# Performance work log

Hardware: AMD Instinct MI355X
Metric: run time of the kernel (lower is better)

The kernel has to match this reference:

```python
import jax, jax.numpy as jnp
import numpy as np

N_NODES = 100000

def gcn_conv(x, W, b, src, dst):
    n = x.shape[0]
    loop = jnp.arange(n, dtype=src.dtype)
    src_f = jnp.concatenate([src, loop])
    dst_f = jnp.concatenate([dst, loop])
    deg = jax.ops.segment_sum(jnp.ones_like(src_f, dtype=x.dtype), dst_f, num_segments=n)
    dinv = jnp.where(deg > 0, deg ** -0.5, 0.0)
    norm = dinv[src_f] * dinv[dst_f]              # [E+N]
    h = x @ W                                      # [N, out]
    msg = h[src_f] * norm[:, None]                 # gather + scale
    out = jax.ops.segment_sum(msg, dst_f, num_segments=n)
    return out + b

def setup_inputs() -> dict:
    key = jax.random.key(0)
    k1, k2, k3, k4, k5 = jax.random.split(key, 5)
    d = 128
    x = jax.random.normal(k1, (N_NODES, d), dtype=jnp.float32)
    e = jax.random.randint(k2, (2, 3200000), 0, N_NODES, dtype=jnp.int64)
    # Glorot-style init as in PyG GCNConv
    W1 = jax.random.normal(k3, (d, 64), dtype=jnp.float32) * (1.0 / np.sqrt(d))
    b1 = jnp.zeros((64,), dtype=jnp.float32)
    W2 = jax.random.normal(k4, (64, 1), dtype=jnp.float32) * (1.0 / np.sqrt(64))
    b2 = jnp.zeros((1,), dtype=jnp.float32)
    return {"x": x, "e": e, "W1": W1, "b1": b1, "W2": W2, "b2": b2}

def reference(x, e, W1, b1, W2, b2):
    src, dst = e[0], e[1]
    h = jax.nn.relu(gcn_conv(x, W1, b1, src, dst))
    return gcn_conv(h, W2, b2, src, dst)
```

## Files before the change

### kernel.cpp

```cpp
#include <hip/hip_runtime.h>
#include <hip/hip_bf16.h>


typedef short s8_t __attribute__((ext_vector_type(8)));
typedef float f4_t __attribute__((ext_vector_type(4)));

__device__ __forceinline__ float bf2f(unsigned short u) {
    union { unsigned int u; float f; } c; c.u = ((unsigned int)u) << 16; return c.f;
}
__device__ __forceinline__ unsigned short f2bf(float f) {
    union { float f; unsigned int u; } c; c.f = f;
    unsigned int u = c.u;
    unsigned int r = (u + 0x7fffu + ((u >> 16) & 1u)) >> 16;
    return (unsigned short)r;
}
__device__ __forceinline__ float loadF(const void* p, int i, int isbf) {
    return isbf ? bf2f(((const unsigned short*)p)[i]) : ((const float*)p)[i];
}
__device__ __forceinline__ int edgeIdx(const void* e, long long i, int is64) {
    return is64 ? (int)((const long long*)e)[i] : ((const int*)e)[i];
}

__global__ void k_detect_prep(const void* e, const void* x, const void* W1,
                              int* flags, unsigned short* __restrict__ wT,
                              unsigned short* __restrict__ wTh,
                              unsigned short* __restrict__ wTl) {
    __shared__ int sfl;
    int tid = threadIdx.x;
    if (tid < 64) {
        unsigned int ew = ((const unsigned int*)e)[2 * tid + 1];
        unsigned long long nz = __ballot(ew != 0);
        unsigned int xw = ((const unsigned int*)x)[tid];
        unsigned int low = xw & 0xffffu;
        unsigned int e8 = (low >> 7) & 0xffu;
        bool plaus = (low == 0u) || (e8 >= 110u && e8 <= 135u);
        unsigned long long pl = __ballot(plaus);
        if (tid == 0) {
            flags[0] = (nz == 0ull) ? 1 : 0;
            int isbf = (__popcll(pl) > 32) ? 1 : 0;
            flags[1] = isbf;
            sfl = isbf;
        }
    }
    __syncthreads();
    int isbf = sfl;
    if (isbf) {
        const unsigned short* w = (const unsigned short*)W1;
        for (int idx = tid; idx < 128 * 64; idx += 256) {
            int k = idx >> 6, n = idx & 63;
            wT[n * 128 + k] = w[idx];
        }
    } else {
        const float* w = (const float*)W1;
        for (int idx = tid; idx < 128 * 64; idx += 256) {
            int k = idx >> 6, n = idx & 63;
            float v = w[idx];
            unsigned short h = f2bf(v);
            wTh[n * 128 + k] = h;
            wTl[n * 128 + k] = f2bf(v - bf2f(h));
        }
    }
}

__launch_bounds__(256)
__global__ void k_hist(const void* e, int* __restrict__ histT, const int* flags,
                       int E, int B, int HB) {
    __shared__ int hist[1024];
    int tid = threadIdx.x;
    int is64 = flags[0];
    for (int f = tid; f < B; f += 256) hist[f] = 0;
    __syncthreads();
    int base = blockIdx.x * 4096;
    #pragma unroll
    for (int k = 0; k < 16; ++k) {
        int i = base + k * 256 + tid;
        if (i < E) {
            int d = edgeIdx(e, (long long)E + i, is64);
            atomicAdd(&hist[d >> 9], 1);
        }
    }
    __syncthreads();
    for (int f = tid; f < B; f += 256)
        histT[(long long)f * HB + blockIdx.x] = hist[f];
}

__global__ void k_scanA(int* __restrict__ data, int* __restrict__ partial, int M) {
    __shared__ int s[256];
    int tid = threadIdx.x;
    int i = blockIdx.x * 256 + tid;
    int v = (i < M) ? data[i] : 0;
    s[tid] = v; __syncthreads();
    for (int off = 1; off < 256; off <<= 1) {
        int t = (tid >= off) ? s[tid - off] : 0;
        __syncthreads(); s[tid] += t; __syncthreads();
    }
    if (i < M) data[i] = s[tid] - v;
    if (tid == 255) partial[blockIdx.x] = s[255];
}

__global__ void k_scanC(int* __restrict__ data, const int* __restrict__ partial,
                        int* __restrict__ bucketStart, int M, int HB, int B, int E) {
    __shared__ int red[256];
    int tid = threadIdx.x;
    int bb = blockIdx.x;
    int s = 0;
    for (int j = tid; j < bb; j += 256) s += partial[j];
    red[tid] = s; __syncthreads();
    for (int off = 128; off > 0; off >>= 1) {
        if (tid < off) red[tid] += red[tid + off];
        __syncthreads();
    }
    int base = red[0];
    int f = bb * 256 + tid;
    if (f < M) {
        int val = data[f] + base;
        data[f] = val;
        int q = f / HB;
        if (f - q * HB == 0) bucketStart[q] = val;
    }
    if (f == 0) bucketStart[B] = E;
}

__launch_bounds__(256)
__global__ void k_part(const void* e, const int* __restrict__ histT,
                       int* __restrict__ part, const int* flags,
                       int E, int B, int HB) {
    __shared__ int lcur[1024];
    __shared__ int lcnt[1024];
    __shared__ int sc[256];
    __shared__ int buf[4096];
    __shared__ unsigned short bkt[4096];
    int tid = threadIdx.x;
    int is64 = flags[0];
    for (int f = tid; f < 1024; f += 256) {
        lcur[f] = (f < B) ? histT[(long long)f * HB + blockIdx.x] : 0;
        lcnt[f] = 0;
    }
    __syncthreads();
    int base = blockIdx.x * 4096;
    int val[16], bk[16], rk[16];
    #pragma unroll
    for (int k = 0; k < 16; ++k) {
        int i = base + k * 256 + tid;
        if (i < E) {
            int s = edgeIdx(e, i, is64);
            int d = edgeIdx(e, (long long)E + i, is64);
            val[k] = s | ((d & 511) << 17);
            bk[k] = d >> 9;
            rk[k] = atomicAdd(&lcnt[bk[k]], 1);
        } else {
            bk[k] = -1;
        }
    }
    __syncthreads();
    int c0 = lcnt[4 * tid], c1 = lcnt[4 * tid + 1];
    int c2 = lcnt[4 * tid + 2], c3 = lcnt[4 * tid + 3];
    int tot = c0 + c1 + c2 + c3;
    sc[tid] = tot; __syncthreads();
    for (int off = 1; off < 256; off <<= 1) {
        int t = (tid >= off) ? sc[tid - off] : 0;
        __syncthreads(); sc[tid] += t; __syncthreads();
    }
    int run = sc[tid] - tot;
    lcnt[4 * tid]     = run;
    lcnt[4 * tid + 1] = run + c0;
    lcnt[4 * tid + 2] = run + c0 + c1;
    lcnt[4 * tid + 3] = run + c0 + c1 + c2;
    __syncthreads();
    #pragma unroll
    for (int k = 0; k < 16; ++k) {
        if (bk[k] >= 0) {
            int slot = lcnt[bk[k]] + rk[k];
            buf[slot] = val[k];
            bkt[slot] = (unsigned short)bk[k];
        }
    }
    __syncthreads();
    int total = E - base; if (total > 4096) total = 4096;
    for (int t = tid; t < total; t += 256) {
        int bb = bkt[t];
        part[lcur[bb] + (t - lcnt[bb])] = buf[t];
    }
}

__launch_bounds__(512)
__global__ void k_sort2(const int* __restrict__ part, const int* __restrict__ bucketStart,
                        int* __restrict__ srcSorted, int* __restrict__ start,
                        float* __restrict__ dinv, int N, int B) {
    __shared__ int cnt[512];
    __shared__ int s[512];
    __shared__ int cur[512];
    int tid = threadIdx.x, b = blockIdx.x;
    cnt[tid] = 0;
    __syncthreads();
    int lo = bucketStart[b], hi = bucketStart[b + 1];
    for (int idx = lo + tid; idx < hi; idx += 512)
        atomicAdd(&cnt[(part[idx] >> 17) & 511], 1);
    __syncthreads();
    int v = cnt[tid];
    s[tid] = v; __syncthreads();
    for (int off = 1; off < 512; off <<= 1) {
        int t = (tid >= off) ? s[tid - off] : 0;
        __syncthreads(); s[tid] += t; __syncthreads();
    }
    int base_ = lo + s[tid] - v;
    cur[tid] = base_;
    int node = b * 512 + tid;
    if (node < N) {
        start[node] = base_;
        dinv[node] = rsqrtf((float)(v + 1));
    }
    if (b == 0 && tid == 0) start[N] = bucketStart[B];
    __syncthreads();
    for (int idx = lo + tid; idx < hi; idx += 512) {
        int pw = part[idx];
        int pos = atomicAdd(&cur[(pw >> 17) & 511], 1);
        srcSorted[pos] = pw & 0x1FFFF;
    }
}

__launch_bounds__(256)
__global__ void k_gemm(const void* x, const unsigned short* __restrict__ wT,
                       const unsigned short* __restrict__ wTh,
                       const unsigned short* __restrict__ wTl,
                       const float* __restrict__ dinv,
                       unsigned short* __restrict__ hb, const int* flags, int N) {
    int tid = threadIdx.x;
    int lane = tid & 63, wv = tid >> 6;
    int q = lane >> 4, r = lane & 15;
    int gw = blockIdx.x * 4 + wv;
    int nW = gridDim.x * 4;
    int RB = (N + 15) >> 4;
    int isbf = flags[1];
    if (isbf) {
        const unsigned short* xb = (const unsigned short*)x;
        for (int rb = gw; rb < RB; rb += nW) {
            int row0 = rb * 16;
            int arow = row0 + r;
            s8_t a[4];
            #pragma unroll
            for (int kk = 0; kk < 4; ++kk)
                a[kk] = (arow < N)
                    ? *(const s8_t*)&xb[(long long)arow * 128 + kk * 32 + q * 8]
                    : (s8_t)(short)0;
            f4_t acc[4];
            #pragma unroll
            for (int nt = 0; nt < 4; ++nt) acc[nt] = (f4_t){0.f, 0.f, 0.f, 0.f};
            #pragma unroll
            for (int nt = 0; nt < 4; ++nt) {
                #pragma unroll
                for (int kk = 0; kk < 4; ++kk) {
                    s8_t b = *(const s8_t*)&wT[(nt * 16 + r) * 128 + kk * 32 + q * 8];
                    acc[nt] = __builtin_amdgcn_mfma_f32_16x16x32_bf16(a[kk], b, acc[nt], 0, 0, 0);
                }
            }
            #pragma unroll
            for (int reg = 0; reg < 4; ++reg) {
                int row = row0 + q * 4 + reg;
                if (row < N) {
                    float dv = dinv[row];
                    #pragma unroll
                    for (int nt = 0; nt < 4; ++nt)
                        hb[(long long)row * 64 + nt * 16 + r] = f2bf(acc[nt][reg] * dv);
                }
            }
        }
    } else {
        const float* xf = (const float*)x;
        f4_t cx0[4], cx1[4];
        int rb = gw;
        if (rb < RB) {
            int arow = rb * 16 + r;
            #pragma unroll
            for (int kk = 0; kk < 4; ++kk) {
                if (arow < N) {
                    const float* p = &xf[(long long)arow * 128 + kk * 32 + q * 8];
                    cx0[kk] = *(const f4_t*)p;
                    cx1[kk] = *(const f4_t*)(p + 4);
                } else {
                    cx0[kk] = (f4_t){0.f, 0.f, 0.f, 0.f};
                    cx1[kk] = (f4_t){0.f, 0.f, 0.f, 0.f};
                }
            }
        }
        for (; rb < RB; rb += nW) {
            s8_t ah[4], al[4];
            #pragma unroll
            for (int kk = 0; kk < 4; ++kk) {
                #pragma unroll
                for (int j = 0; j < 4; ++j) {
                    union { float f; unsigned int u; } c0, h0, r0, c1, h1, r1;
                    c0.f = cx0[kk][j];
                    h0.u = c0.u & 0xffff0000u;
                    ah[kk][j] = (short)(c0.u >> 16);
                    r0.f = c0.f - h0.f;
                    al[kk][j] = (short)(r0.u >> 16);
                    c1.f = cx1[kk][j];
                    h1.u = c1.u & 0xffff0000u;
                    ah[kk][4 + j] = (short)(c1.u >> 16);
                    r1.f = c1.f - h1.f;
                    al[kk][4 + j] = (short)(r1.u >> 16);
                }
            }
            int rbn = rb + nW;
            if (rbn < RB) {
                int arow = rbn * 16 + r;
                #pragma unroll
                for (int kk = 0; kk < 4; ++kk) {
                    if (arow < N) {
                        const float* p = &xf[(long long)arow * 128 + kk * 32 + q * 8];
                        cx0[kk] = *(const f4_t*)p;
                        cx1[kk] = *(const f4_t*)(p + 4);
                    } else {
                        cx0[kk] = (f4_t){0.f, 0.f, 0.f, 0.f};
                        cx1[kk] = (f4_t){0.f, 0.f, 0.f, 0.f};
                    }
                }
            }
            f4_t acc[4];
            #pragma unroll
            for (int nt = 0; nt < 4; ++nt) acc[nt] = (f4_t){0.f, 0.f, 0.f, 0.f};
            #pragma unroll
            for (int nt = 0; nt < 4; ++nt) {
                #pragma unroll
                for (int kk = 0; kk < 4; ++kk) {
                    s8_t bh = *(const s8_t*)&wTh[(nt * 16 + r) * 128 + kk * 32 + q * 8];
                    s8_t bl = *(const s8_t*)&wTl[(nt * 16 + r) * 128 + kk * 32 + q * 8];
                    acc[nt] = __builtin_amdgcn_mfma_f32_16x16x32_bf16(ah[kk], bh, acc[nt], 0, 0, 0);
                    acc[nt] = __builtin_amdgcn_mfma_f32_16x16x32_bf16(al[kk], bh, acc[nt], 0, 0, 0);
                    acc[nt] = __builtin_amdgcn_mfma_f32_16x16x32_bf16(ah[kk], bl, acc[nt], 0, 0, 0);
                }
            }
            int row0 = rb * 16;
            #pragma unroll
            for (int reg = 0; reg < 4; ++reg) {
                int row = row0 + q * 4 + reg;
                if (row < N) {
                    float dv = dinv[row];
                    #pragma unroll
                    for (int nt = 0; nt < 4; ++nt)
                        hb[(long long)row * 64 + nt * 16 + r] = f2bf(acc[nt][reg] * dv);
                }
            }
        }
    }
}

__launch_bounds__(256)
__global__ void k_agg1(const unsigned short* __restrict__ hb,
                       const float* __restrict__ dinv,
                       const int* __restrict__ start,
                       const int* __restrict__ srcSorted,
                       const void* b1, const void* W2, float* __restrict__ sbuf2,
                       const int* flags, int N) {
    int lane = threadIdx.x & 63;
    int node = (blockIdx.x * blockDim.x + threadIdx.x) >> 6;
    if (node >= N) return;
    int isbf = flags[1];
    float di = dinv[node];
    int base = start[node], cnt = start[node + 1] - base;
    float acc = bf2f(hb[(long long)node * 64 + lane]);
    for (int c = 0; c < cnt; c += 64) {
        int t = c + lane;
        int sidx = (t < cnt) ? srcSorted[base + t] : 0;
        int m = cnt - c; if (m > 64) m = 64;
        int t2 = 0;
        for (; t2 + 16 <= m; t2 += 16) {
            int s0  = __shfl(sidx, t2 + 0),  s1  = __shfl(sidx, t2 + 1);
            int s2  = __shfl(sidx, t2 + 2),  s3  = __shfl(sidx, t2 + 3);
            int s4  = __shfl(sidx, t2 + 4),  s5  = __shfl(sidx, t2 + 5);
            int s6  = __shfl(sidx, t2 + 6),  s7  = __shfl(sidx, t2 + 7);
            int s8  = __shfl(sidx, t2 + 8),  s9  = __shfl(sidx, t2 + 9);
            int s10 = __shfl(sidx, t2 + 10), s11 = __shfl(sidx, t2 + 11);
            int s12 = __shfl(sidx, t2 + 12), s13 = __shfl(sidx, t2 + 13);
            int s14 = __shfl(sidx, t2 + 14), s15 = __shfl(sidx, t2 + 15);
            unsigned short v0  = hb[(long long)s0  * 64 + lane];
            unsigned short v1  = hb[(long long)s1  * 64 + lane];
            unsigned short v2  = hb[(long long)s2  * 64 + lane];
            unsigned short v3  = hb[(long long)s3  * 64 + lane];
            unsigned short v4  = hb[(long long)s4  * 64 + lane];
            unsigned short v5  = hb[(long long)s5  * 64 + lane];
            unsigned short v6  = hb[(long long)s6  * 64 + lane];
            unsigned short v7  = hb[(long long)s7  * 64 + lane];
            unsigned short v8  = hb[(long long)s8  * 64 + lane];
            unsigned short v9  = hb[(long long)s9  * 64 + lane];
            unsigned short v10 = hb[(long long)s10 * 64 + lane];
            unsigned short v11 = hb[(long long)s11 * 64 + lane];
            unsigned short v12 = hb[(long long)s12 * 64 + lane];
            unsigned short v13 = hb[(long long)s13 * 64 + lane];
            unsigned short v14 = hb[(long long)s14 * 64 + lane];
            unsigned short v15 = hb[(long long)s15 * 64 + lane];
            acc += bf2f(v0);  acc += bf2f(v1);  acc += bf2f(v2);  acc += bf2f(v3);
            acc += bf2f(v4);  acc += bf2f(v5);  acc += bf2f(v6);  acc += bf2f(v7);
            acc += bf2f(v8);  acc += bf2f(v9);  acc += bf2f(v10); acc += bf2f(v11);
            acc += bf2f(v12); acc += bf2f(v13); acc += bf2f(v14); acc += bf2f(v15);
        }
        for (; t2 + 8 <= m; t2 += 8) {
            int s0 = __shfl(sidx, t2 + 0), s1 = __shfl(sidx, t2 + 1);
            int s2 = __shfl(sidx, t2 + 2), s3 = __shfl(sidx, t2 + 3);
            int s4 = __shfl(sidx, t2 + 4), s5 = __shfl(sidx, t2 + 5);
            int s6 = __shfl(sidx, t2 + 6), s7 = __shfl(sidx, t2 + 7);
            unsigned short v0 = hb[(long long)s0 * 64 + lane];
            unsigned short v1 = hb[(long long)s1 * 64 + lane];
            unsigned short v2 = hb[(long long)s2 * 64 + lane];
            unsigned short v3 = hb[(long long)s3 * 64 + lane];
            unsigned short v4 = hb[(long long)s4 * 64 + lane];
            unsigned short v5 = hb[(long long)s5 * 64 + lane];
            unsigned short v6 = hb[(long long)s6 * 64 + lane];
            unsigned short v7 = hb[(long long)s7 * 64 + lane];
            acc += bf2f(v0); acc += bf2f(v1); acc += bf2f(v2); acc += bf2f(v3);
            acc += bf2f(v4); acc += bf2f(v5); acc += bf2f(v6); acc += bf2f(v7);
        }
        for (; t2 < m; ++t2) {
            int s0 = __shfl(sidx, t2);
            acc += bf2f(hb[(long long)s0 * 64 + lane]);
        }
    }
    float v = acc * di + loadF(b1, lane, isbf);
    v = fmaxf(v, 0.f);
    float p = v * loadF(W2, lane, isbf);
    #pragma unroll
    for (int o = 32; o >= 1; o >>= 1) p += __shfl_xor(p, o);
    if (lane == 0) sbuf2[node] = p * di;
}

__launch_bounds__(256)
__global__ void k_agg2(const float* __restrict__ sbuf2, const float* __restrict__ dinv,
                       const int* __restrict__ start,
                       const int* __restrict__ srcSorted,
                       const void* b2, void* out, const int* flags, int N) {
    int lane = threadIdx.x & 63;
    int node = (blockIdx.x * blockDim.x + threadIdx.x) >> 6;
    if (node >= N) return;
    int isbf = flags[1];
    float di = dinv[node];
    int base = start[node], cnt = start[node + 1] - base;
    float part = 0.f;
    for (int t = lane; t < cnt; t += 64) part += sbuf2[srcSorted[base + t]];
    #pragma unroll
    for (int o = 32; o >= 1; o >>= 1) part += __shfl_xor(part, o);
    if (lane == 0) {
        float o_ = (part + sbuf2[node]) * di + loadF(b2, 0, isbf);
        if (isbf) ((unsigned short*)out)[node] = f2bf(o_);
        else      ((float*)out)[node] = o_;
    }
}

extern "C" void kernel_launch(void* const* d_in, const int* in_sizes, int n_in,
                              void* d_out, int out_size, void* d_ws, size_t ws_size,
                              hipStream_t stream) {
    const void* x  = d_in[0];
    const void* e  = d_in[1];
    const void* W1 = d_in[2];
    const void* b1 = d_in[3];
    const void* W2 = d_in[4];
    const void* b2 = d_in[5];
    int N = in_sizes[0] / 128;
    int E = in_sizes[1] / 2;
    int B  = (N + 511) / 512;
    int HB = (E + 4095) / 4096;
    int M  = B * HB;
    int nP = (M + 255) / 256;
    int NB = B * 512;
    int EP = ((E + 255) / 256) * 256;

    int*   wsI         = (int*)d_ws;
    int*   flags       = wsI;
    unsigned short* wT  = (unsigned short*)(wsI + 256);
    unsigned short* wTh = (unsigned short*)(wsI + 256 + 4096);
    unsigned short* wTl = (unsigned short*)(wsI + 256 + 8192);
    int*   histT       = wsI + 256 + 12288;
    int*   partial     = histT + ((M + 255) / 256) * 256;
    int*   bucketStart = partial + ((nP + 255) / 256) * 256;
    float* dinv        = (float*)(bucketStart + 1040);
    float* sbuf2       = dinv + NB;
    int*   start       = (int*)(sbuf2 + NB);
    int*   srcSorted   = start + NB + 256;
    int*   part        = srcSorted + EP;
    unsigned short* hb = (unsigned short*)part;

    hipLaunchKernelGGL(k_detect_prep, dim3(1), dim3(256), 0, stream,
                       e, x, W1, flags, wT, wTh, wTl);
    hipLaunchKernelGGL(k_hist, dim3(HB), dim3(256), 0, stream, e, histT, flags, E, B, HB);
    hipLaunchKernelGGL(k_scanA, dim3(nP), dim3(256), 0, stream, histT, partial, M);
    hipLaunchKernelGGL(k_scanC, dim3(nP), dim3(256), 0, stream,
                       histT, partial, bucketStart, M, HB, B, E);
    hipLaunchKernelGGL(k_part, dim3(HB), dim3(256), 0, stream, e, histT, part, flags, E, B, HB);
    hipLaunchKernelGGL(k_sort2, dim3(B), dim3(512), 0, stream,
                       part, bucketStart, srcSorted, start, dinv, N, B);
    hipLaunchKernelGGL(k_gemm, dim3(512), dim3(256), 0, stream,
                       x, wT, wTh, wTl, dinv, hb, flags, N);
    hipLaunchKernelGGL(k_agg1, dim3((N + 3) / 4), dim3(256), 0, stream,
                       hb, dinv, start, srcSorted, b1, W2, sbuf2, flags, N);
    hipLaunchKernelGGL(k_agg2, dim3((N + 3) / 4), dim3(256), 0, stream,
                       sbuf2, dinv, start, srcSorted, b2, d_out, flags, N);
}
```

Measured before the change: 297.8 us.

## Replace global histogram+scan partition with local-sorted chunks and binary-search gather

Removes the separate histogram pass over dst and the two-kernel global scan. Each partition block now sorts its 4096-edge chunk by bucket locally, writes it back in place, and records per-bucket offsets and counts. A per-bucket reduction produces bucket totals, and the sort kernel binary-searches the chunk offsets to gather its bucket's edges from every chunk. This avoids one full read of the edge array and two launches, but the sort kernel now does scattered reads with a binary search over about 782 chunks per element, twice.

```diff
diff --git a/kernel.cpp b/kernel.cpp
--- a/kernel.cpp
+++ b/kernel.cpp
@@ -63,79 +63,15 @@
 }
 
 __launch_bounds__(256)
-__global__ void k_hist(const void* e, int* __restrict__ histT, const int* flags,
-                       int E, int B, int HB) {
-    __shared__ int hist[1024];
-    int tid = threadIdx.x;
-    int is64 = flags[0];
-    for (int f = tid; f < B; f += 256) hist[f] = 0;
-    __syncthreads();
-    int base = blockIdx.x * 4096;
-    #pragma unroll
-    for (int k = 0; k < 16; ++k) {
-        int i = base + k * 256 + tid;
-        if (i < E) {
-            int d = edgeIdx(e, (long long)E + i, is64);
-            atomicAdd(&hist[d >> 9], 1);
-        }
-    }
-    __syncthreads();
-    for (int f = tid; f < B; f += 256)
-        histT[(long long)f * HB + blockIdx.x] = hist[f];
-}
-
-__global__ void k_scanA(int* __restrict__ data, int* __restrict__ partial, int M) {
-    __shared__ int s[256];
-    int tid = threadIdx.x;
-    int i = blockIdx.x * 256 + tid;
-    int v = (i < M) ? data[i] : 0;
-    s[tid] = v; __syncthreads();
-    for (int off = 1; off < 256; off <<= 1) {
-        int t = (tid >= off) ? s[tid - off] : 0;
-        __syncthreads(); s[tid] += t; __syncthreads();
-    }
-    if (i < M) data[i] = s[tid] - v;
-    if (tid == 255) partial[blockIdx.x] = s[255];
-}
-
-__global__ void k_scanC(int* __restrict__ data, const int* __restrict__ partial,
-                        int* __restrict__ bucketStart, int M, int HB, int B, int E) {
-    __shared__ int red[256];
-    int tid = threadIdx.x;
-    int bb = blockIdx.x;
-    int s = 0;
-    for (int j = tid; j < bb; j += 256) s += partial[j];
-    red[tid] = s; __syncthreads();
-    for (int off = 128; off > 0; off >>= 1) {
-        if (tid < off) red[tid] += red[tid + off];
-        __syncthreads();
-    }
-    int base = red[0];
-    int f = bb * 256 + tid;
-    if (f < M) {
-        int val = data[f] + base;
-        data[f] = val;
-        int q = f / HB;
-        if (f - q * HB == 0) bucketStart[q] = val;
-    }
-    if (f == 0) bucketStart[B] = E;
-}
-
-__launch_bounds__(256)
-__global__ void k_part(const void* e, const int* __restrict__ histT,
-                       int* __restrict__ part, const int* flags,
-                       int E, int B, int HB) {
-    __shared__ int lcur[1024];
+__global__ void k_part2(const void* e, int* __restrict__ histT,
+                        int* __restrict__ histC, int* __restrict__ part,
+                        const int* flags, int E, int B, int HB) {
     __shared__ int lcnt[1024];
     __shared__ int sc[256];
     __shared__ int buf[4096];
-    __shared__ unsigned short bkt[4096];
     int tid = threadIdx.x;
     int is64 = flags[0];
-    for (int f = tid; f < 1024; f += 256) {
-        lcur[f] = (f < B) ? histT[(long long)f * HB + blockIdx.x] : 0;
-        lcnt[f] = 0;
-    }
+    for (int f = tid; f < 1024; f += 256) lcnt[f] = 0;
     __syncthreads();
     int base = blockIdx.x * 4096;
     int val[16], bk[16], rk[16];
@@ -168,34 +104,80 @@
     lcnt[4 * tid + 3] = run + c0 + c1 + c2;
     __syncthreads();
     #pragma unroll
-    for (int k = 0; k < 16; ++k) {
-        if (bk[k] >= 0) {
-            int slot = lcnt[bk[k]] + rk[k];
-            buf[slot] = val[k];
-            bkt[slot] = (unsigned short)bk[k];
-        }
-    }
-    __syncthreads();
+    for (int k = 0; k < 16; ++k)
+        if (bk[k] >= 0) buf[lcnt[bk[k]] + rk[k]] = val[k];
+    __syncthreads();
+    for (int f = tid; f < B; f += 256) {
+        int st = lcnt[f], en = lcnt[f + 1];
+        histT[(long long)f * HB + blockIdx.x] = st;
+        histC[(long long)f * HB + blockIdx.x] = en - st;
+    }
     int total = E - base; if (total > 4096) total = 4096;
-    for (int t = tid; t < total; t += 256) {
-        int bb = bkt[t];
-        part[lcur[bb] + (t - lcnt[bb])] = buf[t];
-    }
+    for (int t = tid; t < total; t += 256) part[base + t] = buf[t];
+}
+
+__launch_bounds__(256)
+__global__ void k_bstart(const int* __restrict__ histC,
+                         int* __restrict__ bucketTotal, int HB) {
+    __shared__ int red[256];
+    int tid = threadIdx.x, b = blockIdx.x;
+    int s = 0;
+    for (int j = tid; j < HB; j += 256) s += histC[(long long)b * HB + j];
+    red[tid] = s; __syncthreads();
+    for (int off = 128; off > 0; off >>= 1) {
+        if (tid < off) red[tid] += red[tid + off];
+        __syncthreads();
+    }
+    if (tid == 0) bucketTotal[b] = red[0];
 }
 
 __launch_bounds__(512)
-__global__ void k_sort2(const int* __restrict__ part, const int* __restrict__ bucketStart,
+__global__ void k_sort2(const int* __restrict__ part, const int* __restrict__ histT,
+                        const int* __restrict__ histC,
+                        const int* __restrict__ bucketTotal,
                         int* __restrict__ srcSorted, int* __restrict__ start,
-                        float* __restrict__ dinv, int N, int B) {
+                        float* __restrict__ dinv, int N, int B, int HB, int E) {
     __shared__ int cnt[512];
     __shared__ int s[512];
     __shared__ int cur[512];
+    __shared__ int Sj[1024];
+    __shared__ int Pj[1024];
     int tid = threadIdx.x, b = blockIdx.x;
+    int ls = 0;
+    for (int j = tid; j < b; j += 512) ls += bucketTotal[j];
+    cnt[tid] = ls; __syncthreads();
+    for (int off = 256; off > 0; off >>= 1) {
+        if (tid < off) cnt[tid] += cnt[tid + off];
+        __syncthreads();
+    }
+    int lo = cnt[0];
+    __syncthreads();
+    for (int j = tid; j < 1024; j += 512) {
+        Sj[j] = (j < HB) ? histT[(long long)b * HB + j] : 0;
+        Pj[j] = (j < HB) ? histC[(long long)b * HB + j] : 0;
+    }
+    __syncthreads();
+    int e0 = Pj[2 * tid], e1 = Pj[2 * tid + 1];
+    int t2 = e0 + e1;
+    s[tid] = t2; __syncthreads();
+    for (int off = 1; off < 512; off <<= 1) {
+        int t = (tid >= off) ? s[tid - off] : 0;
+        __syncthreads(); s[tid] += t; __syncthreads();
+    }
+    int total = s[511];
+    int runp = s[tid] - t2;
+    Pj[2 * tid] = runp; Pj[2 * tid + 1] = runp + e0;
     cnt[tid] = 0;
     __syncthreads();
-    int lo = bucketStart[b], hi = bucketStart[b + 1];
-    for (int idx = lo + tid; idx < hi; idx += 512)
-        atomicAdd(&cnt[(part[idx] >> 17) & 511], 1);
+    for (int k = tid; k < total; k += 512) {
+        int lo2 = 0, hi2 = HB - 1;
+        while (lo2 < hi2) {
+            int mid = (lo2 + hi2 + 1) >> 1;
+            if (Pj[mid] <= k) lo2 = mid; else hi2 = mid - 1;
+        }
+        int pw = part[lo2 * 4096 + Sj[lo2] + (k - Pj[lo2])];
+        atomicAdd(&cnt[(pw >> 17) & 511], 1);
+    }
     __syncthreads();
     int v = cnt[tid];
     s[tid] = v; __syncthreads();
@@ -210,10 +192,15 @@
         start[node] = base_;
         dinv[node] = rsqrtf((float)(v + 1));
     }
-    if (b == 0 && tid == 0) start[N] = bucketStart[B];
-    __syncthreads();
-    for (int idx = lo + tid; idx < hi; idx += 512) {
-        int pw = part[idx];
+    if (b == 0 && tid == 0) start[N] = E;
+    __syncthreads();
+    for (int k = tid; k < total; k += 512) {
+        int lo2 = 0, hi2 = HB - 1;
+        while (lo2 < hi2) {
+            int mid = (lo2 + hi2 + 1) >> 1;
+            if (Pj[mid] <= k) lo2 = mid; else hi2 = mid - 1;
+        }
+        int pw = part[lo2 * 4096 + Sj[lo2] + (k - Pj[lo2])];
         int pos = atomicAdd(&cur[(pw >> 17) & 511], 1);
         srcSorted[pos] = pw & 0x1FFFF;
     }
@@ -460,7 +447,7 @@
     int B  = (N + 511) / 512;
     int HB = (E + 4095) / 4096;
     int M  = B * HB;
-    int nP = (M + 255) / 256;
+    int Mr = ((M + 255) / 256) * 256;
     int NB = B * 512;
     int EP = ((E + 255) / 256) * 256;
 
@@ -470,9 +457,9 @@
     unsigned short* wTh = (unsigned short*)(wsI + 256 + 4096);
     unsigned short* wTl = (unsigned short*)(wsI + 256 + 8192);
     int*   histT       = wsI + 256 + 12288;
-    int*   partial     = histT + ((M + 255) / 256) * 256;
-    int*   bucketStart = partial + ((nP + 255) / 256) * 256;
-    float* dinv        = (float*)(bucketStart + 1040);
+    int*   histC       = histT + Mr;
+    int*   bucketTotal = histC + Mr;
+    float* dinv        = (float*)(bucketTotal + 256);
     float* sbuf2       = dinv + NB;
     int*   start       = (int*)(sbuf2 + NB);
     int*   srcSorted   = start + NB + 256;
@@ -481,13 +468,13 @@
 
     hipLaunchKernelGGL(k_detect_prep, dim3(1), dim3(256), 0, stream,
                        e, x, W1, flags, wT, wTh, wTl);
-    hipLaunchKernelGGL(k_hist, dim3(HB), dim3(256), 0, stream, e, histT, flags, E, B, HB);
-    hipLaunchKernelGGL(k_scanA, dim3(nP), dim3(256), 0, stream, histT, partial, M);
-    hipLaunchKernelGGL(k_scanC, dim3(nP), dim3(256), 0, stream,
-                       histT, partial, bucketStart, M, HB, B, E);
-    hipLaunchKernelGGL(k_part, dim3(HB), dim3(256), 0, stream, e, histT, part, flags, E, B, HB);
+    hipLaunchKernelGGL(k_part2, dim3(HB), dim3(256), 0, stream,
+                       e, histT, histC, part, flags, E, B, HB);
+    hipLaunchKernelGGL(k_bstart, dim3(B), dim3(256), 0, stream,
+                       histC, bucketTotal, HB);
     hipLaunchKernelGGL(k_sort2, dim3(B), dim3(512), 0, stream,
-                       part, bucketStart, srcSorted, start, dinv, N, B);
+                       part, histT, histC, bucketTotal,
+                       srcSorted, start, dinv, N, B, HB, E);
     hipLaunchKernelGGL(k_gemm, dim3(512), dim3(256), 0, stream,
                        x, wT, wTh, wTl, dinv, hb, flags, N);
     hipLaunchKernelGGL(k_agg1, dim3((N + 3) / 4), dim3(256), 0, stream,
```

Result: slower. 314.9 us (+5.7%).
